# Kernel optimization log

Measured on AMD Instinct MI355X. Metric: run time of the kernel, lower is better.

Reference implementation:

```python
import jax, jax.numpy as jnp
import numpy as np

N_NODES = 100000
N_EDGES = 3200000
F_IN = 128
F_HID = 32
F_OUT = 40


def gcn_conv(x, edge_index, edge_weight, W, b):
    # GCNConv with normalize=False: linear transform, then edge-weighted
    # gather from source nodes and scatter-add into destination nodes.
    h = x @ W                                   # [N, F_out]
    src, dst = edge_index[0], edge_index[1]
    msgs = h[src] * edge_weight[:, None]        # [E, F_out] gather + scale
    agg = jax.ops.segment_sum(msgs, dst, num_segments=N_NODES)
    return agg + b


def setup_inputs() -> dict:
    key = jax.random.key(0)
    k1, k2, k3, k4, k5, k6, k7 = jax.random.split(key, 7)
    x = jax.random.normal(k1, (N_NODES, F_IN), dtype=jnp.float32)
    edge_index = jax.random.randint(k2, (2, N_EDGES), 0, N_NODES, dtype=jnp.int64)
    edge_weight = jax.random.uniform(k3, (N_EDGES,), dtype=jnp.float32)
    # Glorot-style init for layer weights, zeros for biases (PyG defaults)
    W1 = jax.random.normal(k4, (F_IN, F_HID), dtype=jnp.float32) * (1.0 / np.sqrt(F_IN))
    b1 = jnp.zeros((F_HID,), dtype=jnp.float32)
    W2 = jax.random.normal(k5, (F_HID, F_OUT), dtype=jnp.float32) * (1.0 / np.sqrt(F_HID))
    b2 = jnp.zeros((F_OUT,), dtype=jnp.float32)
    return {"x": x, "edge_index": edge_index, "edge_weight": edge_weight,
            "W1": W1, "b1": b1, "W2": W2, "b2": b2}


def reference(x, edge_index, edge_weight, W1, b1, W2, b2):
    h = gcn_conv(x, edge_index, edge_weight, W1, b1)
    h = jax.nn.relu(h)
    # F.dropout(training=self.training) is identity in eval mode
    h = gcn_conv(h, edge_index, edge_weight, W2, b2)
    return jax.nn.log_softmax(h, axis=1)
```

## Files before the change

kernel.cpp:

```cpp
#include <hip/hip_runtime.h>
#include <hip/hip_fp16.h>
#include <math.h>

#define N_NODES 100000
#define N_EDGES 3200000
#define F_IN    128
#define F_HID   32
#define F_OUT   40
#define NBINS   ((N_NODES + 255) >> 8)
#define EPB     4096
#define NBLK    ((N_EDGES + EPB - 1) / EPB)
#define BKT_CAP (N_EDGES + 8 * N_NODES)

typedef _Float16 h2_t __attribute__((ext_vector_type(2)));
__device__ __forceinline__ float fdot2u(unsigned a, unsigned b, float c) {
    return __builtin_amdgcn_fdot2(__builtin_bit_cast(h2_t, a),
                                  __builtin_bit_cast(h2_t, b), c, false);
}

__global__ __launch_bounds__(256) void gemm1_kernel(const float* __restrict__ x,
                                                    const float* __restrict__ W,
                                                    __half* __restrict__ h1h) {
    __shared__ float Ws[F_IN * F_HID];
    __shared__ float Xs[32][F_IN + 4];
    const int tid  = threadIdx.x;
    const int row0 = blockIdx.x * 32;

    for (int i = tid; i < (F_IN * F_HID) / 4; i += 256)
        ((float4*)Ws)[i] = ((const float4*)W)[i];

    for (int i = tid; i < 1024; i += 256) {
        int r = i >> 5;
        int c = i & 31;
        ((float4*)&Xs[r][0])[c] = ((const float4*)x)[(size_t)(row0 + r) * (F_IN / 4) + c];
    }
    __syncthreads();

    const int r  = tid >> 3;
    const int c0 = (tid & 7) * 4;
    float a0 = 0.f, a1 = 0.f, a2 = 0.f, a3 = 0.f;
    for (int k = 0; k < F_IN; ++k) {
        const float xv = Xs[r][k];
        const float* wrow = &Ws[k * F_HID + c0];
        a0 += xv * wrow[0];
        a1 += xv * wrow[1];
        a2 += xv * wrow[2];
        a3 += xv * wrow[3];
    }
    const int row = row0 + r;
    __half2* o = (__half2*)(h1h + (size_t)row * F_HID + c0);
    o[0] = __floats2half2_rn(a0, a1);
    o[1] = __floats2half2_rn(a2, a3);
}

__global__ __launch_bounds__(256) void histA_kernel(const int* __restrict__ ei,
                                                    int* __restrict__ gcnt) {
    __shared__ int lh[NBINS];
    const int tid = threadIdx.x;
    const int e0  = blockIdx.x * EPB;
    for (int i = tid; i < NBINS; i += 256) lh[i] = 0;
    __syncthreads();

    for (int base = 0; base < EPB; base += 1024) {
        const int e = e0 + base + 4 * tid;
        if (e + 3 < N_EDGES) {
            const int4 dv = *(const int4*)&ei[N_EDGES + e];
            atomicAdd(&lh[dv.x >> 8], 1);
            atomicAdd(&lh[dv.y >> 8], 1);
            atomicAdd(&lh[dv.z >> 8], 1);
            atomicAdd(&lh[dv.w >> 8], 1);
        } else {
            for (int k = 0; k < 4; ++k)
                if (e + k < N_EDGES) atomicAdd(&lh[ei[N_EDGES + e + k] >> 8], 1);
        }
    }
    __syncthreads();
    for (int b = tid; b < NBINS; b += 256)
        gcnt[(size_t)blockIdx.x * NBINS + b] = lh[b];
}

__global__ __launch_bounds__(256) void colscan_kernel(const int* __restrict__ gcnt,
                                                      int* __restrict__ pbase,
                                                      int* __restrict__ bintot) {
    __shared__ int s[256];
    __shared__ int carry;
    const int b   = blockIdx.x;
    const int tid = threadIdx.x;
    if (tid == 0) carry = 0;
    __syncthreads();
    for (int c = 0; c < NBLK; c += 256) {
        const int blk = c + tid;
        const int v = (blk < NBLK) ? gcnt[(size_t)blk * NBINS + b] : 0;
        s[tid] = v;
        __syncthreads();
        for (int off = 1; off < 256; off <<= 1) {
            int u = (tid >= off) ? s[tid - off] : 0;
            __syncthreads();
            s[tid] += u;
            __syncthreads();
        }
        if (blk < NBLK) pbase[(size_t)blk * NBINS + b] = carry + s[tid] - v;
        __syncthreads();
        if (tid == 255) carry += s[255];
        __syncthreads();
    }
    if (tid == 0) bintot[b] = carry;
}

__global__ __launch_bounds__(512) void binscan_kernel(const int* __restrict__ bintot,
                                                      int* __restrict__ binbase) {
    __shared__ int s[512];
    const int t = threadIdx.x;
    const int v = (t < NBINS) ? bintot[t] : 0;
    s[t] = v;
    __syncthreads();
    for (int off = 1; off < 512; off <<= 1) {
        int u = (t >= off) ? s[t - off] : 0;
        __syncthreads();
        s[t] += u;
        __syncthreads();
    }
    if (t <= NBINS) binbase[t] = s[t] - v;
}

__global__ __launch_bounds__(256) void placeA_kernel(const int* __restrict__ ei,
                                                     const float* __restrict__ ew,
                                                     const int* __restrict__ gcnt,
                                                     const int* __restrict__ binbase,
                                                     const int* __restrict__ pbase,
                                                     int* __restrict__ stg4,
                                                     unsigned char* __restrict__ dlowg) {
    __shared__ int lhist[512];
    __shared__ int lscan[512];
    __shared__ int lcur[512];
    __shared__ int lwbase[512];
    __shared__ int stmp[256];
    __shared__ int lstg4[EPB];
    __shared__ unsigned short lbin[EPB];
    __shared__ unsigned char ldlow[EPB];
    const int tid = threadIdx.x;
    const int blk = blockIdx.x;
    const int e0  = blk * EPB;
    const int tot = min(EPB, N_EDGES - e0);

    lhist[tid] = 0; lhist[tid + 256] = 0;
    lwbase[tid] = 0; lwbase[tid + 256] = 0;
    __syncthreads();
    for (int b = tid; b < NBINS; b += 256) {
        lhist[b]  = gcnt[(size_t)blk * NBINS + b];
        lwbase[b] = binbase[b] + pbase[(size_t)blk * NBINS + b];
    }
    __syncthreads();

    const int ca = lhist[2 * tid];
    const int cb = lhist[2 * tid + 1];
    const int pair = ca + cb;
    stmp[tid] = pair;
    __syncthreads();
    for (int off = 1; off < 256; off <<= 1) {
        int u = (tid >= off) ? stmp[tid - off] : 0;
        __syncthreads();
        stmp[tid] += u;
        __syncthreads();
    }
    const int pexcl = stmp[tid] - pair;
    lscan[2 * tid]     = pexcl;
    lscan[2 * tid + 1] = pexcl + ca;
    lcur[2 * tid]      = pexcl;
    lcur[2 * tid + 1]  = pexcl + ca;
    __syncthreads();

#define PLACE1(S, D, WF)                                                        \
    {                                                                           \
        const int b = (D) >> 8;                                                 \
        const int p = atomicAdd(&lcur[b], 1);                                   \
        lstg4[p] = (S) | ((int)__half_as_ushort(__float2half(WF)) << 17);       \
        lbin[p] = (unsigned short)b;                                            \
        ldlow[p] = (unsigned char)((D) & 255);                                  \
    }
    for (int base = 0; base < EPB; base += 1024) {
        const int e = e0 + base + 4 * tid;
        if (e + 3 < N_EDGES) {
            const int4   sv = *(const int4*)&ei[e];
            const int4   dv = *(const int4*)&ei[N_EDGES + e];
            const float4 wv = *(const float4*)&ew[e];
            PLACE1(sv.x, dv.x, wv.x);
            PLACE1(sv.y, dv.y, wv.y);
            PLACE1(sv.z, dv.z, wv.z);
            PLACE1(sv.w, dv.w, wv.w);
        } else {
            for (int k = 0; k < 4; ++k)
                if (e + k < N_EDGES)
                    PLACE1(ei[e + k], ei[N_EDGES + e + k], ew[e + k]);
        }
    }
#undef PLACE1
    __syncthreads();

    for (int i = tid; i < tot; i += 256) {
        const int b = lbin[i];
        const int pos = lwbase[b] + (i - lscan[b]);
        stg4[pos] = lstg4[i];
        dlowg[pos] = ldlow[i];
    }
}

__global__ __launch_bounds__(256) void partB1_kernel(const int* __restrict__ binbase,
                                                     const unsigned char* __restrict__ dlowg,
                                                     int* __restrict__ offsIB,
                                                     int* __restrict__ pbt) {
    __shared__ int lcnt[256];
    __shared__ int lsc[256];
    const int tid   = threadIdx.x;
    const int b     = blockIdx.x;
    const int start = binbase[b];
    const int end   = binbase[b + 1];

    lcnt[tid] = 0;
    __syncthreads();
    for (int j = start + tid; j < end; j += 256)
        atomicAdd(&lcnt[dlowg[j]], 1);
    __syncthreads();

    const int padded = (lcnt[tid] + 7) & ~7;
    lsc[tid] = padded;
    __syncthreads();
    for (int off = 1; off < 256; off <<= 1) {
        int u = (tid >= off) ? lsc[tid - off] : 0;
        __syncthreads();
        lsc[tid] += u;
        __syncthreads();
    }
    offsIB[(b << 8) + tid] = lsc[tid] - padded;
    if (tid == 255) pbt[b] = lsc[255];
}

__global__ __launch_bounds__(512) void padscan_kernel(const int* __restrict__ pbt,
                                                      int* __restrict__ pbb,
                                                      int* __restrict__ offs) {
    __shared__ int s[512];
    const int t = threadIdx.x;
    const int v = (t < NBINS) ? pbt[t] : 0;
    s[t] = v;
    __syncthreads();
    for (int off = 1; off < 512; off <<= 1) {
        int u = (t >= off) ? s[t - off] : 0;
        __syncthreads();
        s[t] += u;
        __syncthreads();
    }
    const int excl = s[t] - v;
    if (t <= NBINS) pbb[t] = excl;
    if (t == NBINS) offs[N_NODES] = excl;
}

__global__ __launch_bounds__(256) void partB2_kernel(const int* __restrict__ binbase,
                                                     const int* __restrict__ stg4,
                                                     const unsigned char* __restrict__ dlowg,
                                                     const int* __restrict__ pbb,
                                                     const int* __restrict__ offsIB,
                                                     int* __restrict__ offs,
                                                     int* __restrict__ bkt) {
    __shared__ int lcur[256];
    const int tid  = threadIdx.x;
    const int b    = blockIdx.x;
    const int node = (b << 8) + tid;
    const int base = pbb[b] + offsIB[node];
    const int pend = (tid < 255) ? (pbb[b] + offsIB[node + 1]) : pbb[b + 1];
    lcur[tid] = base;
    if (node < N_NODES) offs[node] = base;
    __syncthreads();

    const int start = binbase[b];
    const int end   = binbase[b + 1];
    for (int j = start + tid; j < end; j += 256) {
        const int word = stg4[j];
        const int pos = atomicAdd(&lcur[dlowg[j]], 1);
        bkt[pos] = word;
    }
    __syncthreads();

    for (int k = lcur[tid]; k < pend; ++k) bkt[k] = 0;
}

__device__ __forceinline__ void gather_acc(const int* __restrict__ bkt,
                                           int j, const int jend,
                                           const char* __restrict__ tbl,
                                           const unsigned sub8, const int g,
                                           float& a0, float& a1, float& a2, float& a3) {
#define PAIR_BODY(PX, PY, RA, RB)                                               \
    {                                                                           \
        const unsigned wp = __builtin_amdgcn_perm((unsigned)(PY) >> 17,         \
                                                  (unsigned)(PX) >> 17,         \
                                                  0x05040100u);                 \
        a0 = fdot2u(__builtin_amdgcn_perm((RB).x, (RA).x, 0x05040100u), wp, a0);\
        a1 = fdot2u(__builtin_amdgcn_perm((RB).x, (RA).x, 0x07060302u), wp, a1);\
        a2 = fdot2u(__builtin_amdgcn_perm((RB).y, (RA).y, 0x05040100u), wp, a2);\
        a3 = fdot2u(__builtin_amdgcn_perm((RB).y, (RA).y, 0x07060302u), wp, a3);\
    }
#define TBL(P) (*(const uint2*)(tbl + (((unsigned)(P) & 0x1FFFFu) << 6) + sub8))
    for (; j + 64 <= jend; j += 64) {
        const int4 pq0 = *(const int4*)&bkt[j + 4 * g];
        const int4 pq1 = *(const int4*)&bkt[j + 32 + 4 * g];
        const uint2 r0 = TBL(pq0.x);
        const uint2 r1 = TBL(pq0.y);
        const uint2 r2 = TBL(pq0.z);
        const uint2 r3 = TBL(pq0.w);
        const uint2 r4 = TBL(pq1.x);
        const uint2 r5 = TBL(pq1.y);
        const uint2 r6 = TBL(pq1.z);
        const uint2 r7 = TBL(pq1.w);
        PAIR_BODY(pq0.x, pq0.y, r0, r1);
        PAIR_BODY(pq0.z, pq0.w, r2, r3);
        PAIR_BODY(pq1.x, pq1.y, r4, r5);
        PAIR_BODY(pq1.z, pq1.w, r6, r7);
    }
    if (j + 32 <= jend) {
        const int4 pq = *(const int4*)&bkt[j + 4 * g];
        const uint2 r0 = TBL(pq.x);
        const uint2 r1 = TBL(pq.y);
        const uint2 r2 = TBL(pq.z);
        const uint2 r3 = TBL(pq.w);
        PAIR_BODY(pq.x, pq.y, r0, r1);
        PAIR_BODY(pq.z, pq.w, r2, r3);
        j += 32;
    }
    if (j + 16 <= jend) {
        const int2 pp = *(const int2*)&bkt[j + 2 * g];
        const uint2 r0 = TBL(pp.x);
        const uint2 r1 = TBL(pp.y);
        PAIR_BODY(pp.x, pp.y, r0, r1);
        j += 16;
    }
    if (j < jend) {
        const unsigned p = (unsigned)bkt[j + g];
        const unsigned w = p >> 17;
        const uint2 rv = TBL(p);
        a0 = fdot2u(rv.x & 0xFFFFu, w, a0);
        a1 = fdot2u(rv.x >> 16,     w, a1);
        a2 = fdot2u(rv.y & 0xFFFFu, w, a2);
        a3 = fdot2u(rv.y >> 16,     w, a3);
    }
#undef TBL
#undef PAIR_BODY
}

__global__ __launch_bounds__(256) void gather1_kernel(const int* __restrict__ offs,
                                                      const int* __restrict__ bkt,
                                                      const __half* __restrict__ h1h,
                                                      const float* __restrict__ b1,
                                                      __half* __restrict__ rh) {
    const int wave = threadIdx.x >> 6, lane = threadIdx.x & 63;
    const int node = blockIdx.x * 4 + wave;
    const int g    = lane >> 3;
    const int sub  = lane & 7;
    const unsigned sub8 = sub * 8;

    float a0 = 0.f, a1 = 0.f, a2 = 0.f, a3 = 0.f;
    gather_acc(bkt, offs[node], offs[node + 1], (const char*)h1h, sub8, g,
               a0, a1, a2, a3);
    #pragma unroll
    for (int off = 8; off < 64; off <<= 1) {
        a0 += __shfl_xor(a0, off);
        a1 += __shfl_xor(a1, off);
        a2 += __shfl_xor(a2, off);
        a3 += __shfl_xor(a3, off);
    }
    if (g == 0) {
        const float4 bb = ((const float4*)b1)[sub];
        a0 = fmaxf(a0 + bb.x, 0.f);
        a1 = fmaxf(a1 + bb.y, 0.f);
        a2 = fmaxf(a2 + bb.z, 0.f);
        a3 = fmaxf(a3 + bb.w, 0.f);
        uint2 o;
        *(__half2*)&o.x = __floats2half2_rn(a0, a1);
        *(__half2*)&o.y = __floats2half2_rn(a2, a3);
        *(uint2*)((char*)rh + (size_t)node * 64 + sub8) = o;
    }
}

__global__ __launch_bounds__(256) void gather2_lsm_kernel(const int* __restrict__ offs,
                                                          const int* __restrict__ bkt,
                                                          const __half* __restrict__ rh,
                                                          const float* __restrict__ W2,
                                                          const float* __restrict__ b2,
                                                          float* __restrict__ out) {
    __shared__ float W2s[F_HID * F_OUT];
    __shared__ float rb[4][F_HID];
    const int tid = threadIdx.x;
    for (int i = tid; i < F_HID * F_OUT; i += 256) W2s[i] = W2[i];

    const int wave = tid >> 6, lane = tid & 63;
    const int node = blockIdx.x * 4 + wave;
    const int g    = lane >> 3;
    const int sub  = lane & 7;
    const unsigned sub8 = sub * 8;

    float a0 = 0.f, a1 = 0.f, a2 = 0.f, a3 = 0.f;
    gather_acc(bkt, offs[node], offs[node + 1], (const char*)rh, sub8, g,
               a0, a1, a2, a3);
    #pragma unroll
    for (int off = 8; off < 64; off <<= 1) {
        a0 += __shfl_xor(a0, off);
        a1 += __shfl_xor(a1, off);
        a2 += __shfl_xor(a2, off);
        a3 += __shfl_xor(a3, off);
    }
    if (g == 0)
        ((float4*)&rb[wave][0])[sub] = make_float4(a0, a1, a2, a3);
    __syncthreads();

    float val = -INFINITY;
    if (lane < F_OUT) {
        float acc = b2[lane];
        #pragma unroll
        for (int k = 0; k < F_HID; ++k)
            acc += rb[wave][k] * W2s[k * F_OUT + lane];
        val = acc;
    }
    float m = val;
    for (int off = 32; off; off >>= 1) m = fmaxf(m, __shfl_xor(m, off));
    float ex = (lane < F_OUT) ? __expf(val - m) : 0.f;
    for (int off = 32; off; off >>= 1) ex += __shfl_xor(ex, off);
    if (lane < F_OUT) out[(size_t)node * F_OUT + lane] = val - m - __logf(ex);
}

extern "C" void kernel_launch(void* const* d_in, const int* in_sizes, int n_in,
                              void* d_out, int out_size, void* d_ws, size_t ws_size,
                              hipStream_t stream) {
    const float* x  = (const float*)d_in[0];
    const int*   ei = (const int*)d_in[1];
    const float* ew = (const float*)d_in[2];
    const float* W1 = (const float*)d_in[3];
    const float* b1 = (const float*)d_in[4];
    const float* W2 = (const float*)d_in[5];
    const float* b2 = (const float*)d_in[6];
    float* out = (float*)d_out;

    char* p = (char*)d_ws;
    size_t off = 0;
    auto alloc = [&](size_t bytes) {
        char* r = p + off;
        off += (bytes + 15) & ~(size_t)15;
        return r;
    };
    int*   gcnt    = (int*)  alloc((size_t)NBLK * NBINS * 4);
    int*   pbase   = (int*)  alloc((size_t)NBLK * NBINS * 4);
    int*   bintot  = (int*)  alloc((size_t)NBINS * 4);
    int*   binbase = (int*)  alloc((size_t)(NBINS + 1) * 4);
    int*   pbt     = (int*)  alloc((size_t)NBINS * 4);
    int*   pbb     = (int*)  alloc((size_t)(NBINS + 1) * 4);
    int*   offsIB  = (int*)  alloc((size_t)NBINS * 256 * 4);
    int*   offs    = (int*)  alloc((size_t)(N_NODES + 1) * 4);
    int*   bkt     = (int*)  alloc((size_t)BKT_CAP * 4);
    char*  uni     = (char*) alloc((size_t)N_EDGES * 5);
    int*   stg4    = (int*)uni;
    unsigned char* dlowg = (unsigned char*)(uni + (size_t)N_EDGES * 4);
    __half* h1h    = (__half*)uni;
    __half* rh     = h1h + (size_t)N_NODES * F_HID;

    histA_kernel<<<NBLK, 256, 0, stream>>>(ei, gcnt);
    colscan_kernel<<<NBINS, 256, 0, stream>>>(gcnt, pbase, bintot);
    binscan_kernel<<<1, 512, 0, stream>>>(bintot, binbase);
    placeA_kernel<<<NBLK, 256, 0, stream>>>(ei, ew, gcnt, binbase, pbase, stg4, dlowg);
    partB1_kernel<<<NBINS, 256, 0, stream>>>(binbase, dlowg, offsIB, pbt);
    padscan_kernel<<<1, 512, 0, stream>>>(pbt, pbb, offs);
    partB2_kernel<<<NBINS, 256, 0, stream>>>(binbase, stg4, dlowg, pbb, offsIB, offs, bkt);

    gemm1_kernel<<<N_NODES / 32, 256, 0, stream>>>(x, W1, h1h);
    gather1_kernel<<<N_NODES / 4, 256, 0, stream>>>(offs, bkt, h1h, b1, rh);

    gather2_lsm_kernel<<<N_NODES / 4, 256, 0, stream>>>(offs, bkt, rh, W2, b2, out);
}
```

Baseline: 214.7 us.

## Map one node per 8-lane group in gathers and split log-softmax into own kernel

The gather kernels now give each node an 8-lane group instead of a full 64-lane wave, with each lane walking the whole padded edge list in chunks of 8. This drops the cross-group shuffle reduction and the lanes left idle on low-degree nodes. The second gather writes raw aggregates to a new workspace buffer, and a separate kernel applies W2, bias and log-softmax. The trade-offs are an extra launch and a global round trip of the hidden aggregates, and high-degree nodes now take longer per group. The loop reads 8 entries per step, so it relies on bucket segments being padded to multiples of 8.

```diff
diff --git a/kernel.cpp b/kernel.cpp
--- a/kernel.cpp
+++ b/kernel.cpp
@@ -283,10 +283,10 @@
     for (int k = lcur[tid]; k < pend; ++k) bkt[k] = 0;
 }
 
-__device__ __forceinline__ void gather_acc(const int* __restrict__ bkt,
+__device__ __forceinline__ void gather_grp(const int* __restrict__ bkt,
                                            int j, const int jend,
                                            const char* __restrict__ tbl,
-                                           const unsigned sub8, const int g,
+                                           const unsigned sub8,
                                            float& a0, float& a1, float& a2, float& a3) {
 #define PAIR_BODY(PX, PY, RA, RB)                                               \
     {                                                                           \
@@ -299,47 +299,21 @@
         a3 = fdot2u(__builtin_amdgcn_perm((RB).y, (RA).y, 0x07060302u), wp, a3);\
     }
 #define TBL(P) (*(const uint2*)(tbl + (((unsigned)(P) & 0x1FFFFu) << 6) + sub8))
-    for (; j + 64 <= jend; j += 64) {
-        const int4 pq0 = *(const int4*)&bkt[j + 4 * g];
-        const int4 pq1 = *(const int4*)&bkt[j + 32 + 4 * g];
-        const uint2 r0 = TBL(pq0.x);
-        const uint2 r1 = TBL(pq0.y);
-        const uint2 r2 = TBL(pq0.z);
-        const uint2 r3 = TBL(pq0.w);
-        const uint2 r4 = TBL(pq1.x);
-        const uint2 r5 = TBL(pq1.y);
-        const uint2 r6 = TBL(pq1.z);
-        const uint2 r7 = TBL(pq1.w);
-        PAIR_BODY(pq0.x, pq0.y, r0, r1);
-        PAIR_BODY(pq0.z, pq0.w, r2, r3);
-        PAIR_BODY(pq1.x, pq1.y, r4, r5);
-        PAIR_BODY(pq1.z, pq1.w, r6, r7);
-    }
-    if (j + 32 <= jend) {
-        const int4 pq = *(const int4*)&bkt[j + 4 * g];
-        const uint2 r0 = TBL(pq.x);
-        const uint2 r1 = TBL(pq.y);
-        const uint2 r2 = TBL(pq.z);
-        const uint2 r3 = TBL(pq.w);
-        PAIR_BODY(pq.x, pq.y, r0, r1);
-        PAIR_BODY(pq.z, pq.w, r2, r3);
-        j += 32;
-    }
-    if (j + 16 <= jend) {
-        const int2 pp = *(const int2*)&bkt[j + 2 * g];
-        const uint2 r0 = TBL(pp.x);
-        const uint2 r1 = TBL(pp.y);
-        PAIR_BODY(pp.x, pp.y, r0, r1);
-        j += 16;
-    }
-    if (j < jend) {
-        const unsigned p = (unsigned)bkt[j + g];
-        const unsigned w = p >> 17;
-        const uint2 rv = TBL(p);
-        a0 = fdot2u(rv.x & 0xFFFFu, w, a0);
-        a1 = fdot2u(rv.x >> 16,     w, a1);
-        a2 = fdot2u(rv.y & 0xFFFFu, w, a2);
-        a3 = fdot2u(rv.y >> 16,     w, a3);
+    for (; j < jend; j += 8) {
+        const int4 p0 = *(const int4*)&bkt[j];
+        const int4 p1 = *(const int4*)&bkt[j + 4];
+        const uint2 r0 = TBL(p0.x);
+        const uint2 r1 = TBL(p0.y);
+        const uint2 r2 = TBL(p0.z);
+        const uint2 r3 = TBL(p0.w);
+        const uint2 r4 = TBL(p1.x);
+        const uint2 r5 = TBL(p1.y);
+        const uint2 r6 = TBL(p1.z);
+        const uint2 r7 = TBL(p1.w);
+        PAIR_BODY(p0.x, p0.y, r0, r1);
+        PAIR_BODY(p0.z, p0.w, r2, r3);
+        PAIR_BODY(p1.x, p1.y, r4, r5);
+        PAIR_BODY(p1.z, p1.w, r6, r7);
     }
 #undef TBL
 #undef PAIR_BODY
@@ -350,65 +324,55 @@
                                                       const __half* __restrict__ h1h,
                                                       const float* __restrict__ b1,
                                                       __half* __restrict__ rh) {
-    const int wave = threadIdx.x >> 6, lane = threadIdx.x & 63;
-    const int node = blockIdx.x * 4 + wave;
-    const int g    = lane >> 3;
-    const int sub  = lane & 7;
+    const int tid  = threadIdx.x;
+    const int node = blockIdx.x * 32 + (tid >> 3);
+    const int sub  = tid & 7;
     const unsigned sub8 = sub * 8;
 
     float a0 = 0.f, a1 = 0.f, a2 = 0.f, a3 = 0.f;
-    gather_acc(bkt, offs[node], offs[node + 1], (const char*)h1h, sub8, g,
+    gather_grp(bkt, offs[node], offs[node + 1], (const char*)h1h, sub8,
                a0, a1, a2, a3);
-    #pragma unroll
-    for (int off = 8; off < 64; off <<= 1) {
-        a0 += __shfl_xor(a0, off);
-        a1 += __shfl_xor(a1, off);
-        a2 += __shfl_xor(a2, off);
-        a3 += __shfl_xor(a3, off);
-    }
-    if (g == 0) {
-        const float4 bb = ((const float4*)b1)[sub];
-        a0 = fmaxf(a0 + bb.x, 0.f);
-        a1 = fmaxf(a1 + bb.y, 0.f);
-        a2 = fmaxf(a2 + bb.z, 0.f);
-        a3 = fmaxf(a3 + bb.w, 0.f);
-        uint2 o;
-        *(__half2*)&o.x = __floats2half2_rn(a0, a1);
-        *(__half2*)&o.y = __floats2half2_rn(a2, a3);
-        *(uint2*)((char*)rh + (size_t)node * 64 + sub8) = o;
-    }
-}
-
-__global__ __launch_bounds__(256) void gather2_lsm_kernel(const int* __restrict__ offs,
-                                                          const int* __restrict__ bkt,
-                                                          const __half* __restrict__ rh,
-                                                          const float* __restrict__ W2,
-                                                          const float* __restrict__ b2,
-                                                          float* __restrict__ out) {
+
+    const float4 bb = ((const float4*)b1)[sub];
+    a0 = fmaxf(a0 + bb.x, 0.f);
+    a1 = fmaxf(a1 + bb.y, 0.f);
+    a2 = fmaxf(a2 + bb.z, 0.f);
+    a3 = fmaxf(a3 + bb.w, 0.f);
+    uint2 o;
+    *(__half2*)&o.x = __floats2half2_rn(a0, a1);
+    *(__half2*)&o.y = __floats2half2_rn(a2, a3);
+    *(uint2*)((char*)rh + (size_t)node * 64 + sub8) = o;
+}
+
+__global__ __launch_bounds__(256) void gather2_kernel(const int* __restrict__ offs,
+                                                      const int* __restrict__ bkt,
+                                                      const __half* __restrict__ rh,
+                                                      float* __restrict__ sacc) {
+    const int tid  = threadIdx.x;
+    const int node = blockIdx.x * 32 + (tid >> 3);
+    const int sub  = tid & 7;
+    const unsigned sub8 = sub * 8;
+
+    float a0 = 0.f, a1 = 0.f, a2 = 0.f, a3 = 0.f;
+    gather_grp(bkt, offs[node], offs[node + 1], (const char*)rh, sub8,
+               a0, a1, a2, a3);
+
+    ((float4*)sacc)[(size_t)node * 8 + sub] = make_float4(a0, a1, a2, a3);
+}
+
+__global__ __launch_bounds__(256) void lsm_kernel(const float* __restrict__ sacc,
+                                                  const float* __restrict__ W2,
+                                                  const float* __restrict__ b2,
+                                                  float* __restrict__ out) {
     __shared__ float W2s[F_HID * F_OUT];
     __shared__ float rb[4][F_HID];
     const int tid = threadIdx.x;
     for (int i = tid; i < F_HID * F_OUT; i += 256) W2s[i] = W2[i];
+    __syncthreads();
 
     const int wave = tid >> 6, lane = tid & 63;
     const int node = blockIdx.x * 4 + wave;
-    const int g    = lane >> 3;
-    const int sub  = lane & 7;
-    const unsigned sub8 = sub * 8;
-
-    float a0 = 0.f, a1 = 0.f, a2 = 0.f, a3 = 0.f;
-    gather_acc(bkt, offs[node], offs[node + 1], (const char*)rh, sub8, g,
-               a0, a1, a2, a3);
-    #pragma unroll
-    for (int off = 8; off < 64; off <<= 1) {
-        a0 += __shfl_xor(a0, off);
-        a1 += __shfl_xor(a1, off);
-        a2 += __shfl_xor(a2, off);
-        a3 += __shfl_xor(a3, off);
-    }
-    if (g == 0)
-        ((float4*)&rb[wave][0])[sub] = make_float4(a0, a1, a2, a3);
-    __syncthreads();
+    if (lane < F_HID) rb[wave][lane] = sacc[(size_t)node * F_HID + lane];
 
     float val = -INFINITY;
     if (lane < F_OUT) {
@@ -453,6 +417,7 @@
     int*   offsIB  = (int*)  alloc((size_t)NBINS * 256 * 4);
     int*   offs    = (int*)  alloc((size_t)(N_NODES + 1) * 4);
     int*   bkt     = (int*)  alloc((size_t)BKT_CAP * 4);
+    float* sacc    = (float*)alloc((size_t)N_NODES * F_HID * 4);
     char*  uni     = (char*) alloc((size_t)N_EDGES * 5);
     int*   stg4    = (int*)uni;
     unsigned char* dlowg = (unsigned char*)(uni + (size_t)N_EDGES * 4);
@@ -468,7 +433,8 @@
     partB2_kernel<<<NBINS, 256, 0, stream>>>(binbase, stg4, dlowg, pbb, offsIB, offs, bkt);
 
     gemm1_kernel<<<N_NODES / 32, 256, 0, stream>>>(x, W1, h1h);
-    gather1_kernel<<<N_NODES / 4, 256, 0, stream>>>(offs, bkt, h1h, b1, rh);
-
-    gather2_lsm_kernel<<<N_NODES / 4, 256, 0, stream>>>(offs, bkt, rh, W2, b2, out);
-}
+    gather1_kernel<<<N_NODES / 32, 256, 0, stream>>>(offs, bkt, h1h, b1, rh);
+
+    gather2_kernel<<<N_NODES / 32, 256, 0, stream>>>(offs, bkt, rh, sacc);
+    lsm_kernel<<<N_NODES / 4, 256, 0, stream>>>(sacc, W2, b2, out);
+}
```

Measured after the change: 234.0 us. +9.0%, slower.
